# Performance work log

Hardware: AMD Instinct MI355X
Metric: run time of the kernel (lower is better)

## Reference

```python
import jax, jax.numpy as jnp
import numpy as np

D_MODEL = 2048
NUM_HEADS = 16
D_K = D_MODEL // NUM_HEADS


def setup_inputs() -> dict:
    key = jax.random.key(0)
    k_x, k_wqkv, k_bqkv, k_wo, k_bo = jax.random.split(key, 5)
    B, S = 2, 2048
    x = jax.random.normal(k_x, (B, S, D_MODEL), dtype=jnp.float32)
    # torch Linear init scale ~ 1/sqrt(fan_in); stored here as [in, out] for x @ W
    s = 1.0 / np.sqrt(D_MODEL)
    W_qkv = jax.random.uniform(k_wqkv, (D_MODEL, 3 * D_MODEL), minval=-s, maxval=s, dtype=jnp.float32)
    b_qkv = jax.random.uniform(k_bqkv, (3 * D_MODEL,), minval=-s, maxval=s, dtype=jnp.float32)
    W_out = jax.random.uniform(k_wo, (D_MODEL, D_MODEL), minval=-s, maxval=s, dtype=jnp.float32)
    b_out = jax.random.uniform(k_bo, (D_MODEL,), minval=-s, maxval=s, dtype=jnp.float32)
    return {"x": x, "W_qkv": W_qkv, "b_qkv": b_qkv, "W_out": W_out, "b_out": b_out}


def reference(x, W_qkv, b_qkv, W_out, b_out):
    B, S, D = x.shape
    qkv = x @ W_qkv + b_qkv                      # [B, S, 3*D]
    qkv = qkv.reshape(B, S, NUM_HEADS, 3 * D_K).transpose(0, 2, 1, 3)  # [B, H, S, 3*d_k]
    q, k, v = jnp.split(qkv, 3, axis=-1)          # each [B, H, S, d_k]
    scores = jnp.einsum("bhqd,bhkd->bhqk", q, k) / jnp.sqrt(jnp.float32(D_K))
    attn = jax.nn.softmax(scores, axis=-1)        # dropout is identity in eval mode
    out = jnp.einsum("bhqk,bhkd->bhqd", attn, v)  # [B, H, S, d_k]
    out = out.transpose(0, 2, 1, 3).reshape(B, S, D)
    return out @ W_out + b_out
```

## Files before the change

### kernel.cpp

```cpp
#include <hip/hip_runtime.h>
#include <hip/hip_bf16.h>

typedef unsigned short ushort_t;
typedef short short8 __attribute__((ext_vector_type(8)));
typedef short short4v __attribute__((ext_vector_type(4)));
typedef float floatx4 __attribute__((ext_vector_type(4)));

#define MFMA16(a,b,c) __builtin_amdgcn_mfma_f32_16x16x32_bf16((a),(b),(c),0,0,0)

#define D_MODEL 2048
#define NHEAD   16
#define DK      128
#define SEQ     2048
#define BATCH   2

static __device__ __forceinline__ ushort_t f2bf(float f){
  union { float f; unsigned int i; } v; v.f = f;
  unsigned int r = v.i + 0x7FFFu + ((v.i >> 16) & 1u);
  return (ushort_t)(r >> 16);
}

typedef __attribute__((address_space(3))) void       lds_void_t;
typedef __attribute__((address_space(1))) const void gbl_void_t;
#define GLOAD_LDS16(g, l) \
  __builtin_amdgcn_global_load_lds((gbl_void_t*)(g), (lds_void_t*)(l), 16, 0, 0)

__global__ __launch_bounds__(256) void cvt_k(const float* __restrict__ in,
                                             ushort_t* __restrict__ out) {
  int i = (blockIdx.x * 256 + threadIdx.x) * 8;
  floatx4 a = *(const floatx4*)&in[i];
  floatx4 b = *(const floatx4*)&in[i + 4];
  short8 r;
  for (int j = 0; j < 4; ++j) r[j] = (short)f2bf(a[j]);
  for (int j = 0; j < 4; ++j) r[4 + j] = (short)f2bf(b[j]);
  *(short8*)&out[i] = r;
}

__global__ __launch_bounds__(256) void transpose_cvt_k(const float* __restrict__ in,
                                                       ushort_t* __restrict__ out,
                                                       int R, int C) {
  __shared__ ushort_t tile[64][65];
  int tr = blockIdx.y * 64, tc = blockIdx.x * 64;
  int t = threadIdx.x;
  for (int p = 0; p < 16; ++p) {
    int idx = t + p * 256;
    int r = idx >> 6, c = idx & 63;
    tile[r][c] = f2bf(in[(size_t)(tr + r) * C + (tc + c)]);
  }
  __syncthreads();
  for (int p = 0; p < 16; ++p) {
    int idx = t + p * 256;
    int r = idx >> 6, c = idx & 63;
    out[(size_t)(tc + r) * R + (tr + c)] = tile[c][r];
  }
}

template <int MODE>
__global__ __launch_bounds__(512, 1) void gemm8p(const ushort_t* __restrict__ A,
                                                 const ushort_t* __restrict__ BT,
                                                 const float* __restrict__ bias,
                                                 ushort_t* __restrict__ out_q,
                                                 ushort_t* __restrict__ out_k,
                                                 ushort_t* __restrict__ out_v,
                                                 float* __restrict__ outp,
                                                 int N, int nbn) {
  __shared__ __align__(16) ushort_t As[2][128 * 64];
  __shared__ __align__(16) ushort_t Bs[2][256 * 64];

  const int nwg = gridDim.x;
  const int orig = blockIdx.x;
  const int wg = (orig & 7) * (nwg >> 3) + (orig >> 3);
  const int bm = wg / nbn, bn = wg - bm * nbn;
  const int row0 = bm * 128, col0 = bn * 256;

  const int t = threadIdx.x, wave = t >> 6, lane = t & 63;
  const int wm = wave >> 2, wn = wave & 3;
  const int l15 = lane & 15, lg = lane >> 4;
  const int swz = (l15 & 7) << 4;
  const int csrc = ((lane & 7) * 16) ^ ((lane >> 3) << 4);
  const int rsub = lane >> 3;

  char* AsC = (char*)&As[0][0];
  char* BsC = (char*)&Bs[0][0];

  floatx4 acc[4][4];
#pragma unroll
  for (int m = 0; m < 4; ++m)
#pragma unroll
    for (int n = 0; n < 4; ++n) acc[m][n] = (floatx4){0.f, 0.f, 0.f, 0.f};

#define STAGE_A(buf, k0, j) \
  GLOAD_LDS16((const char*)&A[(size_t)(row0 + (j) * 64 + wave * 8 + rsub) * 2048 + (k0)] + csrc, \
              AsC + (buf) * 16384 + ((j) * 64 + wave * 8) * 128)
#define STAGE_B(buf, k0, j) \
  GLOAD_LDS16((const char*)&BT[(size_t)(col0 + (j) * 64 + wave * 8 + rsub) * 2048 + (k0)] + csrc, \
              BsC + (buf) * 32768 + ((j) * 64 + wave * 8) * 128)

  STAGE_A(0, 0, 0); STAGE_A(0, 0, 1);
  STAGE_B(0, 0, 0); STAGE_B(0, 0, 1); STAGE_B(0, 0, 2); STAGE_B(0, 0, 3);
  asm volatile("s_waitcnt vmcnt(0)" ::: "memory");
  __builtin_amdgcn_s_barrier();

  for (int kt = 0; kt < 32; ++kt) {
    const int buf = kt & 1, nb = buf ^ 1;
    const int nk0 = (kt + 1) * 64;
    const char* Ab = AsC + buf * 16384;
    const char* Bb = BsC + buf * 32768;
    short8 a[4], b[4];

#pragma unroll
    for (int m = 0; m < 4; ++m)
      a[m] = *(const short8*)(Ab + (wm * 64 + m * 16 + l15) * 128 + ((lg * 16) ^ swz));
#pragma unroll
    for (int n = 0; n < 4; ++n)
      b[n] = *(const short8*)(Bb + (wn * 64 + n * 16 + l15) * 128 + ((lg * 16) ^ swz));
    if (kt < 31) {
      STAGE_A(nb, nk0, 0); STAGE_A(nb, nk0, 1);
      STAGE_B(nb, nk0, 0); STAGE_B(nb, nk0, 1);
    }
    __builtin_amdgcn_s_barrier();
    asm volatile("s_waitcnt lgkmcnt(0)" ::: "memory");
    __builtin_amdgcn_sched_barrier(0);
    __builtin_amdgcn_s_setprio(1);
#pragma unroll
    for (int m = 0; m < 4; ++m)
#pragma unroll
      for (int n = 0; n < 4; ++n)
        acc[m][n] = MFMA16(a[m], b[n], acc[m][n]);
    __builtin_amdgcn_s_setprio(0);
    __builtin_amdgcn_s_barrier();

#pragma unroll
    for (int m = 0; m < 4; ++m)
      a[m] = *(const short8*)(Ab + (wm * 64 + m * 16 + l15) * 128 + ((64 + lg * 16) ^ swz));
#pragma unroll
    for (int n = 0; n < 4; ++n)
      b[n] = *(const short8*)(Bb + (wn * 64 + n * 16 + l15) * 128 + ((64 + lg * 16) ^ swz));
    if (kt < 31) {
      STAGE_B(nb, nk0, 2); STAGE_B(nb, nk0, 3);
    }
    __builtin_amdgcn_s_barrier();
    asm volatile("s_waitcnt lgkmcnt(0)" ::: "memory");
    __builtin_amdgcn_sched_barrier(0);
    __builtin_amdgcn_s_setprio(1);
#pragma unroll
    for (int m = 0; m < 4; ++m)
#pragma unroll
      for (int n = 0; n < 4; ++n)
        acc[m][n] = MFMA16(a[m], b[n], acc[m][n]);
    __builtin_amdgcn_s_setprio(0);
    asm volatile("s_waitcnt vmcnt(0)" ::: "memory");
    __builtin_amdgcn_s_barrier();
  }
#undef STAGE_A
#undef STAGE_B

  if (MODE == 1) {
#pragma unroll
    for (int m = 0; m < 4; ++m)
#pragma unroll
      for (int n = 0; n < 4; ++n) {
        int c = col0 + wn * 64 + n * 16 + l15;
        float bv = bias[c];
        int r0 = row0 + wm * 64 + m * 16 + lg * 4;
#pragma unroll
        for (int j = 0; j < 4; ++j)
          outp[(size_t)(r0 + j) * N + c] = acc[m][n][j] + bv;
      }
  } else {
#pragma unroll
    for (int m = 0; m < 4; ++m)
#pragma unroll
      for (int n = 0; n < 4; ++n) {
        int c = col0 + wn * 64 + n * 16 + l15;
        float bv = bias[c];
        int blk = c >> 7;
        int h = blk / 3, which = blk - h * 3;
        int d = c & 127;
        int r0 = row0 + wm * 64 + m * 16 + lg * 4;
        int b = r0 >> 11;
        int s0 = r0 & 2047;
        if (which < 2) {
          ushort_t* dst = (which == 0) ? out_q : out_k;
          size_t base = ((size_t)(b * NHEAD + h) * SEQ) * DK;
#pragma unroll
          for (int j = 0; j < 4; ++j)
            dst[base + (size_t)(s0 + j) * DK + d] = f2bf(acc[m][n][j] + bv);
        } else {
          size_t base = ((size_t)(b * NHEAD + h) * DK + d) * SEQ + s0;
          short4v tmp;
#pragma unroll
          for (int j = 0; j < 4; ++j) tmp[j] = (short)f2bf(acc[m][n][j] + bv);
          *(short4v*)&out_v[base] = tmp;
        }
      }
  }
}

__global__ __launch_bounds__(256, 2) void attn_k(const ushort_t* __restrict__ qws,
                                                 const ushort_t* __restrict__ kws,
                                                 const ushort_t* __restrict__ vtws,
                                                 ushort_t* __restrict__ ctx) {
  __shared__ __align__(16) ushort_t Ks[2][64 * 128];
  __shared__ __align__(16) ushort_t Vs[2][128 * 64];
  __shared__ __align__(16) ushort_t P[4][32 * 64];

  const int bid = blockIdx.y * gridDim.x + blockIdx.x;
  const int xcd = bid & 7, slot = bid >> 3;
  const int bh = xcd * 4 + (slot & 3);
  const int qt = slot >> 2;
  const int b = bh >> 4, h = bh & 15;
  const int t = threadIdx.x, wave = t >> 6, lane = t & 63;
  const int l15 = lane & 15, lg = lane >> 4;

  const ushort_t* Q  = qws  + (size_t)bh * SEQ * DK;
  const ushort_t* Kp = kws  + (size_t)bh * SEQ * DK;
  const ushort_t* VT = vtws + (size_t)bh * DK * SEQ;

  const int qr = qt * 128 + wave * 32;

  short8 qf[2][4];
#pragma unroll
  for (int m = 0; m < 2; ++m)
#pragma unroll
    for (int kk = 0; kk < 4; ++kk)
      qf[m][kk] = *(const short8*)&Q[(size_t)(qr + m * 16 + l15) * DK + kk * 32 + lg * 8];

  floatx4 o[2][8];
#pragma unroll
  for (int m = 0; m < 2; ++m)
#pragma unroll
    for (int n = 0; n < 8; ++n) o[m][n] = (floatx4){0.f, 0.f, 0.f, 0.f};
  float mrow[2] = {-1e30f, -1e30f};
  float lrowp[2] = {0.f, 0.f};

  char* Pb = (char*)&P[wave][0];
  const int swz = (l15 & 7) << 4;
  const float scale = 0.08838834764831845f;

  auto STAGE = [&](int buf, int kv0) {
#pragma unroll
    for (int t2 = 0; t2 < 4; ++t2) {
      int rowK = wave * 16 + t2 * 4 + (lane >> 4);
      int csK = ((lane & 15) * 16) ^ ((rowK & 7) << 4);
      GLOAD_LDS16((const char*)&Kp[(size_t)(kv0 + rowK) * DK] + csK,
                  (char*)&Ks[buf][0] + wave * 4096 + t2 * 1024);
      int rowV = wave * 32 + t2 * 8 + (lane >> 3);
      int csV = ((lane & 7) * 16) ^ ((rowV & 7) << 4);
      GLOAD_LDS16((const char*)&VT[(size_t)rowV * SEQ + kv0] + csV,
                  (char*)&Vs[buf][0] + wave * 4096 + t2 * 1024);
    }
  };

  STAGE(0, 0);
  __syncthreads();

  for (int it = 0; it < SEQ / 64; ++it) {
    const char* KsC = (const char*)&Ks[it & 1][0];
    const char* VsC = (const char*)&Vs[it & 1][0];
    if (it < SEQ / 64 - 1) STAGE((it + 1) & 1, (it + 1) * 64);

    floatx4 s[2][4];
#pragma unroll
    for (int m = 0; m < 2; ++m)
#pragma unroll
      for (int c = 0; c < 4; ++c) s[m][c] = (floatx4){0.f, 0.f, 0.f, 0.f};
#pragma unroll
    for (int c = 0; c < 4; ++c) {
      short8 kf[4];
#pragma unroll
      for (int kk = 0; kk < 4; ++kk)
        kf[kk] = *(const short8*)(KsC + (c * 16 + l15) * 256 + ((kk * 64 + lg * 16) ^ swz));
#pragma unroll
      for (int m = 0; m < 2; ++m)
#pragma unroll
        for (int kk = 0; kk < 4; ++kk)
          s[m][c] = MFMA16(kf[kk], qf[m][kk], s[m][c]);
    }

#pragma unroll
    for (int m = 0; m < 2; ++m) {
      float tt[4][4];
      float rm = -1e30f;
#pragma unroll
      for (int c = 0; c < 4; ++c)
#pragma unroll
        for (int j = 0; j < 4; ++j) {
          tt[c][j] = s[m][c][j] * scale;
          rm = fmaxf(rm, tt[c][j]);
        }
      rm = fmaxf(rm, __shfl_xor(rm, 16));
      rm = fmaxf(rm, __shfl_xor(rm, 32));

      if (__any(rm > mrow[m] + 8.f)) {
        float rmn = fmaxf(rm, mrow[m]);
        float corr = __expf(mrow[m] - rmn);
        mrow[m] = rmn;
        lrowp[m] *= corr;
        float co[4];
#pragma unroll
        for (int j = 0; j < 4; ++j) co[j] = __shfl(corr, lg * 4 + j);
#pragma unroll
        for (int n = 0; n < 8; ++n)
#pragma unroll
          for (int j = 0; j < 4; ++j) o[m][n][j] *= co[j];
      }

      float psum = 0.f;
#pragma unroll
      for (int c = 0; c < 4; ++c) {
        float p0 = __expf(tt[c][0] - mrow[m]);
        float p1 = __expf(tt[c][1] - mrow[m]);
        float p2 = __expf(tt[c][2] - mrow[m]);
        float p3 = __expf(tt[c][3] - mrow[m]);
        psum += (p0 + p1) + (p2 + p3);
        short4v pk;
        pk[0] = (short)f2bf(p0); pk[1] = (short)f2bf(p1);
        pk[2] = (short)f2bf(p2); pk[3] = (short)f2bf(p3);
        *(short4v*)(Pb + (m * 16 + l15) * 128 + ((c * 32 + lg * 8) ^ swz)) = pk;
      }
      lrowp[m] += psum;
    }

    asm volatile("s_waitcnt lgkmcnt(0)" ::: "memory");
    __builtin_amdgcn_sched_barrier(0);

    short8 pa[2][2];
#pragma unroll
    for (int m = 0; m < 2; ++m)
#pragma unroll
      for (int ch = 0; ch < 2; ++ch)
        pa[m][ch] = *(const short8*)(Pb + (m * 16 + l15) * 128 + ((ch * 64 + lg * 16) ^ swz));
#pragma unroll
    for (int n = 0; n < 8; ++n) {
      short8 v0 = *(const short8*)(VsC + (n * 16 + l15) * 128 + ((lg * 16) ^ swz));
      short8 v1 = *(const short8*)(VsC + (n * 16 + l15) * 128 + ((64 + lg * 16) ^ swz));
#pragma unroll
      for (int m = 0; m < 2; ++m) {
        o[m][n] = MFMA16(pa[m][0], v0, o[m][n]);
        o[m][n] = MFMA16(pa[m][1], v1, o[m][n]);
      }
    }
    __syncthreads();
  }

#pragma unroll
  for (int m = 0; m < 2; ++m) {
    lrowp[m] += __shfl_xor(lrowp[m], 16);
    lrowp[m] += __shfl_xor(lrowp[m], 32);
  }
#pragma unroll
  for (int m = 0; m < 2; ++m) {
    float rcp[4];
#pragma unroll
    for (int j = 0; j < 4; ++j) rcp[j] = 1.f / __shfl(lrowp[m], lg * 4 + j);
#pragma unroll
    for (int n = 0; n < 8; ++n)
#pragma unroll
      for (int j = 0; j < 4; ++j) {
        int row = qr + m * 16 + lg * 4 + j;
        ctx[(size_t)(b * SEQ + row) * D_MODEL + h * DK + n * 16 + l15] =
            f2bf(o[m][n][j] * rcp[j]);
      }
  }
}

extern "C" void kernel_launch(void* const* d_in, const int* in_sizes, int n_in,
                              void* d_out, int out_size, void* d_ws, size_t ws_size,
                              hipStream_t stream) {
  const float* x    = (const float*)d_in[0];
  const float* Wqkv = (const float*)d_in[1];
  const float* bqkv = (const float*)d_in[2];
  const float* Wout = (const float*)d_in[3];
  const float* bout = (const float*)d_in[4];
  float* out = (float*)d_out;

  ushort_t* WqkvT = (ushort_t*)d_ws;
  ushort_t* WoutT = WqkvT + (size_t)6144 * 2048;
  ushort_t* qws   = WoutT + (size_t)2048 * 2048;
  ushort_t* kws   = qws + (size_t)8388608;
  ushort_t* vtws  = kws + (size_t)8388608;
  ushort_t* ctx   = vtws + (size_t)8388608;
  ushort_t* xb    = ctx + (size_t)8388608;

  cvt_k<<<4096, 256, 0, stream>>>(x, xb);
  transpose_cvt_k<<<dim3(6144 / 64, 2048 / 64), 256, 0, stream>>>(Wqkv, WqkvT, 2048, 6144);
  transpose_cvt_k<<<dim3(2048 / 64, 2048 / 64), 256, 0, stream>>>(Wout, WoutT, 2048, 2048);

  gemm8p<0><<<768, 512, 0, stream>>>(xb, WqkvT, bqkv, qws, kws, vtws, nullptr, 6144, 24);
  attn_k<<<dim3(16, 32), 256, 0, stream>>>(qws, kws, vtws, ctx);
  gemm8p<1><<<256, 512, 0, stream>>>(ctx, WoutT, bout, nullptr, nullptr, nullptr, out, 2048, 8);
}
```

Before: 397.5 us.

## Triple-buffer LDS in GEMM to prefetch two k-tiles ahead

Replaces the double-buffered A/B shared tiles with three rotating 48KB buffers and issues global-to-LDS loads two k-iterations ahead. The per-iteration wait becomes vmcnt(6), so one tile's loads can still be in flight while the next is consumed. This is meant to hide global memory latency behind MFMA work, at the cost of 144KB of LDS per block and more complex waitcnt bookkeeping.

```diff
diff --git a/kernel.cpp b/kernel.cpp
--- a/kernel.cpp
+++ b/kernel.cpp
@@ -64,8 +64,7 @@
                                                  ushort_t* __restrict__ out_v,
                                                  float* __restrict__ outp,
                                                  int N, int nbn) {
-  __shared__ __align__(16) ushort_t As[2][128 * 64];
-  __shared__ __align__(16) ushort_t Bs[2][256 * 64];
+  __shared__ __align__(16) ushort_t lds[3 * 24576];
 
   const int nwg = gridDim.x;
   const int orig = blockIdx.x;
@@ -80,8 +79,9 @@
   const int csrc = ((lane & 7) * 16) ^ ((lane >> 3) << 4);
   const int rsub = lane >> 3;
 
-  char* AsC = (char*)&As[0][0];
-  char* BsC = (char*)&Bs[0][0];
+  char* buf0 = (char*)&lds[0];
+  char* buf1 = buf0 + 49152;
+  char* buf2 = buf1 + 49152;
 
   floatx4 acc[4][4];
 #pragma unroll
@@ -89,34 +89,38 @@
 #pragma unroll
     for (int n = 0; n < 4; ++n) acc[m][n] = (floatx4){0.f, 0.f, 0.f, 0.f};
 
-#define STAGE_A(buf, k0, j) \
+#define STAGE_A(dst, k0, j) \
   GLOAD_LDS16((const char*)&A[(size_t)(row0 + (j) * 64 + wave * 8 + rsub) * 2048 + (k0)] + csrc, \
-              AsC + (buf) * 16384 + ((j) * 64 + wave * 8) * 128)
-#define STAGE_B(buf, k0, j) \
+              (dst) + ((j) * 64 + wave * 8) * 128)
+#define STAGE_B(dst, k0, j) \
   GLOAD_LDS16((const char*)&BT[(size_t)(col0 + (j) * 64 + wave * 8 + rsub) * 2048 + (k0)] + csrc, \
-              BsC + (buf) * 32768 + ((j) * 64 + wave * 8) * 128)
-
-  STAGE_A(0, 0, 0); STAGE_A(0, 0, 1);
-  STAGE_B(0, 0, 0); STAGE_B(0, 0, 1); STAGE_B(0, 0, 2); STAGE_B(0, 0, 3);
-  asm volatile("s_waitcnt vmcnt(0)" ::: "memory");
+              (dst) + 16384 + ((j) * 64 + wave * 8) * 128)
+#define STAGE_ALL(dst, k0) \
+  do { STAGE_A(dst, k0, 0); STAGE_A(dst, k0, 1); \
+       STAGE_B(dst, k0, 0); STAGE_B(dst, k0, 1); STAGE_B(dst, k0, 2); STAGE_B(dst, k0, 3); } while (0)
+
+  STAGE_ALL(buf0, 0);
+  STAGE_ALL(buf1, 64);
+  asm volatile("s_waitcnt vmcnt(6)" ::: "memory");
   __builtin_amdgcn_s_barrier();
 
+  char* cur = buf0;
+  char* nxt = buf1;
+  char* stg = buf2;
+
   for (int kt = 0; kt < 32; ++kt) {
-    const int buf = kt & 1, nb = buf ^ 1;
-    const int nk0 = (kt + 1) * 64;
-    const char* Ab = AsC + buf * 16384;
-    const char* Bb = BsC + buf * 32768;
+    const int sk0 = (kt + 2) * 64;
+    const bool stage = (kt < 30);
     short8 a[4], b[4];
 
 #pragma unroll
     for (int m = 0; m < 4; ++m)
-      a[m] = *(const short8*)(Ab + (wm * 64 + m * 16 + l15) * 128 + ((lg * 16) ^ swz));
+      a[m] = *(const short8*)(cur + (wm * 64 + m * 16 + l15) * 128 + ((lg * 16) ^ swz));
 #pragma unroll
     for (int n = 0; n < 4; ++n)
-      b[n] = *(const short8*)(Bb + (wn * 64 + n * 16 + l15) * 128 + ((lg * 16) ^ swz));
-    if (kt < 31) {
-      STAGE_A(nb, nk0, 0); STAGE_A(nb, nk0, 1);
-      STAGE_B(nb, nk0, 0); STAGE_B(nb, nk0, 1);
+      b[n] = *(const short8*)(cur + 16384 + (wn * 64 + n * 16 + l15) * 128 + ((lg * 16) ^ swz));
+    if (stage) {
+      STAGE_A(stg, sk0, 0); STAGE_A(stg, sk0, 1); STAGE_B(stg, sk0, 0);
     }
     __builtin_amdgcn_s_barrier();
     asm volatile("s_waitcnt lgkmcnt(0)" ::: "memory");
@@ -132,12 +136,12 @@
 
 #pragma unroll
     for (int m = 0; m < 4; ++m)
-      a[m] = *(const short8*)(Ab + (wm * 64 + m * 16 + l15) * 128 + ((64 + lg * 16) ^ swz));
+      a[m] = *(const short8*)(cur + (wm * 64 + m * 16 + l15) * 128 + ((64 + lg * 16) ^ swz));
 #pragma unroll
     for (int n = 0; n < 4; ++n)
-      b[n] = *(const short8*)(Bb + (wn * 64 + n * 16 + l15) * 128 + ((64 + lg * 16) ^ swz));
-    if (kt < 31) {
-      STAGE_B(nb, nk0, 2); STAGE_B(nb, nk0, 3);
+      b[n] = *(const short8*)(cur + 16384 + (wn * 64 + n * 16 + l15) * 128 + ((64 + lg * 16) ^ swz));
+    if (stage) {
+      STAGE_B(stg, sk0, 1); STAGE_B(stg, sk0, 2); STAGE_B(stg, sk0, 3);
     }
     __builtin_amdgcn_s_barrier();
     asm volatile("s_waitcnt lgkmcnt(0)" ::: "memory");
@@ -149,11 +153,15 @@
       for (int n = 0; n < 4; ++n)
         acc[m][n] = MFMA16(a[m], b[n], acc[m][n]);
     __builtin_amdgcn_s_setprio(0);
-    asm volatile("s_waitcnt vmcnt(0)" ::: "memory");
+    if (stage) { asm volatile("s_waitcnt vmcnt(6)" ::: "memory"); }
+    else       { asm volatile("s_waitcnt vmcnt(0)" ::: "memory"); }
     __builtin_amdgcn_s_barrier();
+
+    char* old = cur; cur = nxt; nxt = stg; stg = old;
   }
 #undef STAGE_A
 #undef STAGE_B
+#undef STAGE_ALL
 
   if (MODE == 1) {
 #pragma unroll
```

After: 396.7 us. About the same (-0.2%).
